# Kernel tuning notes

Hardware: AMD Instinct MI355X
Metric: run time of the kernel (lower is better)

The kernel has to match this reference:

```python
import jax, jax.numpy as jnp
import numpy as np

NUM_HEADS = 8
N_WIN = 8
TOPK = 4
DIM = 256


def setup_inputs() -> dict:
    key = jax.random.key(0)
    ks = jax.random.split(key, 5)
    B, T, H, W = 16, 16, 16, 16
    N = T * H * W
    x = jax.random.normal(ks[0], (B, N, DIM), dtype=jnp.float32)
    w_qkv = jax.random.normal(ks[1], (DIM, 3 * DIM), dtype=jnp.float32) * (DIM ** -0.5)
    b_qkv = jnp.zeros((3 * DIM,), dtype=jnp.float32)
    w_proj = jax.random.normal(ks[2], (DIM, DIM), dtype=jnp.float32) * (DIM ** -0.5)
    b_proj = jnp.zeros((DIM,), dtype=jnp.float32)
    return {"x": x, "w_qkv": w_qkv, "b_qkv": b_qkv, "w_proj": w_proj,
            "b_proj": b_proj, "T": T, "H": H, "W": W}


def reference(x, w_qkv, b_qkv, w_proj, b_proj, T, H, W):
    B, N, C = x.shape
    h = NUM_HEADS
    d = C // h
    scale = d ** -0.5
    S = H * W

    # qkv projection -> [3, B, T, h, S, d]
    qkv = (x.reshape(B, T, S, C) @ w_qkv + b_qkv).reshape(B, T, S, 3, h, d)
    qkv = jnp.transpose(qkv, (3, 0, 1, 4, 2, 5))
    q, k, v = qkv[0], qkv[1], qkv[2]

    n_win = N_WIN if S % N_WIN == 0 else S
    win = S // n_win
    qr = q.reshape(B, T, h, n_win, win, d)
    kr = k.reshape(B, T, h, n_win, win, d)
    vr = v.reshape(B, T, h, n_win, win, d)

    # spike-driven region features: sum over window tokens
    q_reg = qr.sum(axis=4)  # [B,T,h,n_win,d]
    k_reg = kr.sum(axis=4)
    sim = jnp.einsum('bthnd,bthmd->bthnm', q_reg, k_reg) * scale

    # mask out dead (non-firing) key regions
    activity = jnp.abs(kr).sum(axis=(4, 5))  # [B,T,h,n_win]
    act_mask = (activity > 1e-5).astype(sim.dtype)
    sim = sim + (1.0 - act_mask)[:, :, :, None, :] * -1e9

    tk = min(TOPK, n_win)
    _, idx = jax.lax.top_k(sim, tk)  # [B,T,h,n_win,tk]

    gidx = (idx[..., None] * win + jnp.arange(win)).reshape(B, T, h, n_win, tk * win)

    k_flat = kr.reshape(B, T, h, S, d)
    v_flat = vr.reshape(B, T, h, S, d)
    kg = jnp.take_along_axis(k_flat[:, :, :, None], gidx[..., None], axis=4)
    vg = jnp.take_along_axis(v_flat[:, :, :, None], gidx[..., None], axis=4)

    attn = jnp.einsum('bthnwd,bthngd->bthnwg', qr, kg) * scale
    attn = jax.nn.softmax(attn, axis=-1)
    out = jnp.einsum('bthnwg,bthngd->bthnwd', attn, vg)

    out = out.reshape(B, T, h, S, d).transpose(0, 1, 3, 2, 4).reshape(B, N, C)
    return out @ w_proj + b_proj
```

## Files before the change

### kernel.cpp

```cpp
#include <hip/hip_runtime.h>
#include <math.h>

constexpr int Bn   = 16;
constexpr int Tn   = 16;
constexpr int Sn   = 256;
constexpr int Cn   = 256;
constexpr int NH   = 8;
constexpr int HD   = 32;
constexpr int NW   = 8;
constexpr int WINW = 32;
constexpr float SCALE = 0.17677669529663687f;
constexpr float CEXP  = 0.2550756272475434f;

typedef __attribute__((ext_vector_type(8))) short bf16x8;
typedef __attribute__((ext_vector_type(4))) float f32x4;

__device__ inline float bf2f(unsigned short u) {
  return __uint_as_float(((unsigned int)u) << 16);
}
__device__ inline unsigned short f2bf(float f) {
  unsigned int u = __float_as_uint(f);
  u += 0x7FFFu + ((u >> 16) & 1u);
  return (unsigned short)(u >> 16);
}
__device__ inline unsigned int cvtpk_bf16(float lo, float hi) {
  unsigned int r;
  asm("v_cvt_pk_bf16_f32 %0, %1, %2" : "=v"(r) : "v"(lo), "v"(hi));
  return r;
}
__device__ inline float fast_exp2(float x) {
  float r;
  asm("v_exp_f32 %0, %1" : "=v"(r) : "v"(x));
  return r;
}
__device__ inline void gload16(const void* g, const void* l) {
  __builtin_amdgcn_global_load_lds(
      (const __attribute__((address_space(1))) void*)g,
      (__attribute__((address_space(3))) void*)l, 16, 0, 0);
}

__global__ __launch_bounds__(256) void k_prep(const float* __restrict__ x,
                                              const float* __restrict__ w_qkv,
                                              const float* __restrict__ w_proj,
                                              float* __restrict__ xs,
                                              unsigned short* __restrict__ xb,
                                              unsigned short* __restrict__ wtb,
                                              float* __restrict__ wtf,
                                              unsigned short* __restrict__ wpt) {
  const int blk = blockIdx.x;
  const int tid = threadIdx.x;
  if (blk < 2048) {
    const size_t row0 = (size_t)blk * 32;
    float acc = 0.f;
#pragma unroll
    for (int r = 0; r < 32; ++r) {
      const float val = x[(row0 + r) * Cn + tid];
      acc += val;
      xb[(row0 + r) * Cn + tid] = f2bf(val);
    }
    xs[(size_t)blk * Cn + tid] = acc;
  } else if (blk < 2816) {
    const int co = blk - 2048;
    const float val = w_qkv[(size_t)tid * 768 + co];
    wtf[(size_t)co * 256 + tid] = val;
    wtb[(size_t)co * 256 + tid] = f2bf(val);
  } else {
    const int co = blk - 2816;
    wpt[(size_t)co * 256 + tid] = f2bf(w_proj[(size_t)tid * 256 + co]);
  }
}

__global__ __launch_bounds__(256) void k_reg(const float* __restrict__ xs,
                                             const float* __restrict__ wtf,
                                             const float* __restrict__ bias,
                                             float* __restrict__ reg) {
  __shared__ __align__(16) float As[16][64];
  __shared__ __align__(16) float Bs[16][64];
  const int bx = blockIdx.x;
  const int by = blockIdx.y;
  const int tid = threadIdx.x;
  const int tx = tid & 15, ty = tid >> 4;
  const int row0 = by * 64, col0 = bx * 64;

  float acc[4][4] = {};

  for (int kk0 = 0; kk0 < 256; kk0 += 16) {
    const int m = tid >> 2, ks = (tid & 3) * 4;
    const float4 a4 = *reinterpret_cast<const float4*>(
        xs + (size_t)(row0 + m) * 256 + kk0 + ks);
    As[ks + 0][m] = a4.x; As[ks + 1][m] = a4.y;
    As[ks + 2][m] = a4.z; As[ks + 3][m] = a4.w;
    const float4 b4 = *reinterpret_cast<const float4*>(
        wtf + (size_t)(col0 + m) * 256 + kk0 + ks);
    Bs[ks + 0][m] = b4.x; Bs[ks + 1][m] = b4.y;
    Bs[ks + 2][m] = b4.z; Bs[ks + 3][m] = b4.w;
    __syncthreads();
#pragma unroll
    for (int kk = 0; kk < 16; ++kk) {
      const float4 a = *reinterpret_cast<const float4*>(&As[kk][ty * 4]);
      const float4 b = *reinterpret_cast<const float4*>(&Bs[kk][tx * 4]);
      const float av[4] = {a.x, a.y, a.z, a.w};
      const float bv[4] = {b.x, b.y, b.z, b.w};
#pragma unroll
      for (int i = 0; i < 4; ++i)
#pragma unroll
        for (int j = 0; j < 4; ++j) acc[i][j] = fmaf(av[i], bv[j], acc[i][j]);
    }
    __syncthreads();
  }

  const int colb = col0 + tx * 4;
  const float4 bia = *reinterpret_cast<const float4*>(bias + colb);
#pragma unroll
  for (int i = 0; i < 4; ++i) {
    const int row = row0 + ty * 4 + i;
    float4 o;
    o.x = acc[i][0] + 32.f * bia.x; o.y = acc[i][1] + 32.f * bia.y;
    o.z = acc[i][2] + 32.f * bia.z; o.w = acc[i][3] + 32.f * bia.w;
    *reinterpret_cast<float4*>(reg + (size_t)row * 512 + colb) = o;
  }
}

__global__ __launch_bounds__(64) void k_topk(const float* __restrict__ reg,
                                             int* __restrict__ idxout) {
  __shared__ float sq[8][32];
  __shared__ float sk[8][32];
  __shared__ float sim[8][8];
  const int bth = blockIdx.x;
  const int bt = bth >> 3, h = bth & 7;
  const int t = threadIdx.x;
#pragma unroll
  for (int n = 0; n < 8; ++n) {
    const size_t rb = (size_t)(bt * 8 + n) * 512 + h * 32;
    if (t < 32) sq[n][t] = reg[rb + t];
    else        sk[n][t - 32] = reg[rb + 256 + (t - 32)];
  }
  __syncthreads();
  {
    const int nn = t >> 3, m = t & 7;
    float s = 0.f;
#pragma unroll
    for (int i = 0; i < HD; ++i) s += sq[nn][i] * sk[m][i];
    sim[nn][m] = s;
  }
  __syncthreads();
  if (t < 8) {
    float vals[8];
#pragma unroll
    for (int m = 0; m < 8; ++m) vals[m] = sim[t][m];
#pragma unroll
    for (int j = 0; j < 4; ++j) {
      float best = -3.402823466e38f;
      int bi = 0;
#pragma unroll
      for (int m = 0; m < 8; ++m)
        if (vals[m] > best) { best = vals[m]; bi = m; }
      vals[bi] = -3.402823466e38f;
      idxout[((size_t)bth * 8 + t) * 4 + j] = bi;
    }
  }
}

__global__ __launch_bounds__(256) void k_qkv_mfma(
    const unsigned short* __restrict__ Xb,
    const unsigned short* __restrict__ Wt,
    const float* __restrict__ bias,
    unsigned short* __restrict__ q,
    unsigned short* __restrict__ k,
    unsigned short* __restrict__ v) {
  __shared__ short As[128 * 64];
  __shared__ short Bs[128 * 64];
  const int tid = threadIdx.x;
  const int wid = tid >> 6, lane = tid & 63;
  const int p = blockIdx.x;
  const int bidx = (p & 7) * 384 + (p >> 3);
  const int mt = bidx / 6, nt = bidx - mt * 6;
  const int row0 = mt * 128, col0 = nt * 128;
  const int wm = (wid >> 1) * 64, wn = (wid & 1) * 64;

  f32x4 acc[4][4] = {};

  const int lr = lane >> 3, lc = lane & 7;

  for (int kk0 = 0; kk0 < 256; kk0 += 64) {
#pragma unroll
    for (int j = 0; j < 4; ++j) {
      const int r = wid * 32 + j * 8 + lr;
      const int gsw = (lc ^ (r & 7)) * 8;
      gload16(Xb + (size_t)(row0 + r) * 256 + kk0 + gsw,
              (const char*)As + (wid * 32 + j * 8) * 128);
      gload16(Wt + (size_t)(col0 + r) * 256 + kk0 + gsw,
              (const char*)Bs + (wid * 32 + j * 8) * 128);
    }
    __syncthreads();

#pragma unroll
    for (int ks = 0; ks < 2; ++ks) {
      const int g = ks * 4 + (lane >> 4);
      bf16x8 af[4], bfr[4];
#pragma unroll
      for (int i = 0; i < 4; ++i) {
        const int rm = wm + i * 16 + (lane & 15);
        af[i] = *(const bf16x8*)((const char*)As + rm * 128 + 16 * (g ^ (rm & 7)));
        const int rn = wn + i * 16 + (lane & 15);
        bfr[i] = *(const bf16x8*)((const char*)Bs + rn * 128 + 16 * (g ^ (rn & 7)));
      }
#pragma unroll
      for (int i = 0; i < 4; ++i)
#pragma unroll
        for (int j = 0; j < 4; ++j)
          acc[i][j] = __builtin_amdgcn_mfma_f32_16x16x32_bf16(
              af[i], bfr[j], acc[i][j], 0, 0, 0);
    }
    __syncthreads();
  }

  const int cl = lane & 15, rg = lane >> 4;
#pragma unroll
  for (int j = 0; j < 4; ++j) {
    const int n = col0 + wn + j * 16 + cl;
    const float bia = bias[n];
    const int pp = n >> 8, hh = (n >> 5) & 7, dd = n & 31;
    unsigned short* dst = (pp == 0) ? q : (pp == 1) ? k : v;
#pragma unroll
    for (int i = 0; i < 4; ++i) {
      const int mbase = row0 + wm + i * 16 + rg * 4;
#pragma unroll
      for (int r = 0; r < 4; ++r) {
        const int m = mbase + r;
        const int bt = m >> 8, s = m & 255;
        dst[((size_t)(bt * NH + hh) * Sn + s) * HD + dd] = f2bf(acc[i][j][r] + bia);
      }
    }
  }
}

__global__ __launch_bounds__(256) void k_attn_mfma(
    const unsigned short* __restrict__ qb,
    const unsigned short* __restrict__ kb,
    const unsigned short* __restrict__ vb,
    const int* __restrict__ idx,
    unsigned short* __restrict__ ao) {
  __shared__ __align__(16) short kx[256 * 32];
  __shared__ __align__(16) short vt[32 * 264];
  __shared__ __align__(16) unsigned int pl[4][32 * 35];
  __shared__ float sbuf[4][32];
  const int bth = blockIdx.x;
  const int bt = bth >> 3, h = bth & 7;
  const int tid = threadIdx.x;
  const int wid = tid >> 6, l = tid & 63;
  const int g = l >> 4, q15 = l & 15;
  const unsigned short* kg = kb + (size_t)bth * 8192;
  const unsigned short* vg = vb + (size_t)bth * 8192;
  const unsigned short* qg = qb + (size_t)bth * 8192;

  {
    const int tloc = tid >> 2, cst = tid & 3;
#pragma unroll
    for (int it = 0; it < 4; ++it) {
      const int t = it * 64 + tloc;
      const int csrc = cst ^ ((t >> 1) & 3);
      gload16((const char*)kg + t * 64 + csrc * 16,
              (const char*)kx + it * 4096 + wid * 1024);
    }
  }
  {
    const int t = tid;
    unsigned short us[32];
#pragma unroll
    for (int i = 0; i < 4; ++i)
      *(int4*)(us + 8 * i) = ((const int4*)(vg + (size_t)t * 32))[i];
#pragma unroll
    for (int d = 0; d < 32; ++d) vt[d * 264 + t] = us[d];
  }
  __syncthreads();

#pragma unroll
  for (int ww = 0; ww < 2; ++ww) {
    const int wi = wid + ww * 4;
    const bf16x8 qf0 = *(const bf16x8*)(qg + (wi * 32 + q15) * 32 + g * 8);
    const bf16x8 qf1 = *(const bf16x8*)(qg + (wi * 32 + 16 + q15) * 32 + g * 8);
    const int4 s4 = *(const int4*)(idx + ((size_t)bth * 8 + wi) * 4);
    const int sel[4] = {s4.x, s4.y, s4.z, s4.w};

    f32x4 st[8][2] = {};
    __builtin_amdgcn_s_setprio(1);
#pragma unroll
    for (int mt = 0; mt < 8; ++mt) {
      const int t = sel[mt >> 1] * 32 + (mt & 1) * 16 + q15;
      const bf16x8 kf =
          *(const bf16x8*)((const char*)kx + t * 64 + (g ^ ((t >> 1) & 3)) * 16);
      st[mt][0] = __builtin_amdgcn_mfma_f32_16x16x32_bf16(kf, qf0, st[mt][0], 0, 0, 0);
      st[mt][1] = __builtin_amdgcn_mfma_f32_16x16x32_bf16(kf, qf1, st[mt][1], 0, 0, 0);
    }
    __builtin_amdgcn_s_setprio(0);

    float sm0 = 0.f, sm1 = 0.f;
#pragma unroll
    for (int mt = 0; mt < 8; ++mt)
#pragma unroll
      for (int r = 0; r < 4; ++r) {
        const float e0 = fast_exp2(st[mt][0][r] * CEXP);
        const float e1 = fast_exp2(st[mt][1][r] * CEXP);
        st[mt][0][r] = e0; sm0 += e0;
        st[mt][1][r] = e1; sm1 += e1;
      }
    sm0 += __shfl_xor(sm0, 16); sm0 += __shfl_xor(sm0, 32);
    sm1 += __shfl_xor(sm1, 16); sm1 += __shfl_xor(sm1, 32);
    sbuf[wid][q15] = sm0;
    sbuf[wid][16 + q15] = sm1;

    f32x4 oa[2][2] = {};
#pragma unroll
    for (int c = 0; c < 2; ++c) {
#pragma unroll
      for (int m3 = 0; m3 < 4; ++m3) {
        const int mt = c * 4 + m3;
        const int tl2 = m3 * 8 + 2 * g;
#pragma unroll
        for (int nt = 0; nt < 2; ++nt) {
          const int row = nt * 16 + q15;
          pl[wid][row * 35 + tl2]     = cvtpk_bf16(st[mt][nt][0], st[mt][nt][1]);
          pl[wid][row * 35 + tl2 + 1] = cvtpk_bf16(st[mt][nt][2], st[mt][nt][3]);
        }
      }
      __builtin_amdgcn_s_setprio(1);
#pragma unroll
      for (int a = 0; a < 2; ++a) {
        const bf16x8 pa0 = *(const bf16x8*)((const char*)&pl[wid][0] +
                                            q15 * 140 + (a * 32 + g * 8) * 2);
        const bf16x8 pa1 = *(const bf16x8*)((const char*)&pl[wid][0] +
                                            (16 + q15) * 140 + (a * 32 + g * 8) * 2);
        const int tv = sel[c * 2 + a] * 32 + g * 8;
#pragma unroll
        for (int nt = 0; nt < 2; ++nt) {
          const bf16x8 vf =
              *(const bf16x8*)((const char*)vt + (nt * 16 + q15) * 528 + tv * 2);
          oa[0][nt] = __builtin_amdgcn_mfma_f32_16x16x32_bf16(pa0, vf, oa[0][nt], 0, 0, 0);
          oa[1][nt] = __builtin_amdgcn_mfma_f32_16x16x32_bf16(pa1, vf, oa[1][nt], 0, 0, 0);
        }
      }
      __builtin_amdgcn_s_setprio(0);
    }

    const size_t rowbase = (size_t)bt * 256 + wi * 32;
#pragma unroll
    for (int mtO = 0; mtO < 2; ++mtO) {
      float inv[4];
#pragma unroll
      for (int r = 0; r < 4; ++r)
        inv[r] = __builtin_amdgcn_rcpf(sbuf[wid][mtO * 16 + g * 4 + r]);
#pragma unroll
      for (int nt = 0; nt < 2; ++nt)
#pragma unroll
        for (int r = 0; r < 4; ++r) {
          const size_t tok = rowbase + mtO * 16 + g * 4 + r;
          ao[tok * 256 + h * 32 + nt * 16 + q15] = f2bf(oa[mtO][nt][r] * inv[r]);
        }
    }
  }
}

__global__ __launch_bounds__(256) void k_proj_mfma(
    const unsigned short* __restrict__ AO,
    const unsigned short* __restrict__ Wp,
    const float* __restrict__ bias,
    float* __restrict__ out) {
  __shared__ short As[128 * 64];
  __shared__ short Bs[128 * 64];
  const int tid = threadIdx.x;
  const int wid = tid >> 6, lane = tid & 63;
  const int p = blockIdx.x;
  const int bidx = (p & 7) * 128 + (p >> 3);
  const int mt = bidx >> 1, nt = bidx & 1;
  const int row0 = mt * 128, col0 = nt * 128;
  const int wm = (wid >> 1) * 64, wn = (wid & 1) * 64;

  f32x4 acc[4][4] = {};
  const int lr = lane >> 3, lc = lane & 7;

  for (int kk0 = 0; kk0 < 256; kk0 += 64) {
#pragma unroll
    for (int j = 0; j < 4; ++j) {
      const int r = wid * 32 + j * 8 + lr;
      const int gsw = (lc ^ (r & 7)) * 8;
      gload16(AO + (size_t)(row0 + r) * 256 + kk0 + gsw,
              (const char*)As + (wid * 32 + j * 8) * 128);
      gload16(Wp + (size_t)(col0 + r) * 256 + kk0 + gsw,
              (const char*)Bs + (wid * 32 + j * 8) * 128);
    }
    __syncthreads();

#pragma unroll
    for (int ks = 0; ks < 2; ++ks) {
      const int g = ks * 4 + (lane >> 4);
      bf16x8 af[4], bfr[4];
#pragma unroll
      for (int i = 0; i < 4; ++i) {
        const int rm = wm + i * 16 + (lane & 15);
        af[i] = *(const bf16x8*)((const char*)As + rm * 128 + 16 * (g ^ (rm & 7)));
        const int rn = wn + i * 16 + (lane & 15);
        bfr[i] = *(const bf16x8*)((const char*)Bs + rn * 128 + 16 * (g ^ (rn & 7)));
      }
#pragma unroll
      for (int i = 0; i < 4; ++i)
#pragma unroll
        for (int j = 0; j < 4; ++j)
          acc[i][j] = __builtin_amdgcn_mfma_f32_16x16x32_bf16(
              af[i], bfr[j], acc[i][j], 0, 0, 0);
    }
    __syncthreads();
  }

  const int cl = lane & 15, rg = lane >> 4;
#pragma unroll
  for (int j = 0; j < 4; ++j) {
    const int n = col0 + wn + j * 16 + cl;
    const float bia = bias[n];
#pragma unroll
    for (int i = 0; i < 4; ++i) {
      const int mbase = row0 + wm + i * 16 + rg * 4;
#pragma unroll
      for (int r = 0; r < 4; ++r)
        out[(size_t)(mbase + r) * 256 + n] = acc[i][j][r] + bia;
    }
  }
}

extern "C" void kernel_launch(void* const* d_in, const int* in_sizes, int n_in,
                              void* d_out, int out_size, void* d_ws,
                              size_t ws_size, hipStream_t stream) {
  const float* x      = (const float*)d_in[0];
  const float* w_qkv  = (const float*)d_in[1];
  const float* b_qkv  = (const float*)d_in[2];
  const float* w_proj = (const float*)d_in[3];
  const float* b_proj = (const float*)d_in[4];
  float* out = (float*)d_out;

  char* ws = (char*)d_ws;
  unsigned short* xb  = (unsigned short*)(ws);
  unsigned short* ao  = (unsigned short*)(ws);
  unsigned short* q   = (unsigned short*)(ws + ((size_t)32 << 20));
  unsigned short* k   = (unsigned short*)(ws + ((size_t)64 << 20));
  unsigned short* v   = (unsigned short*)(ws + ((size_t)96 << 20));
  float*          xs  = (float*)(ws + ((size_t)128 << 20));
  unsigned short* wtb = (unsigned short*)(ws + ((size_t)131 << 20));
  unsigned short* wpt = (unsigned short*)(ws + ((size_t)131 << 20) + (512 << 10));
  float*          wtf = (float*)(ws + ((size_t)132 << 20));
  int*            idx = (int*)(ws + ((size_t)133 << 20));
  float*          regf= (float*)(ws + ((size_t)136 << 20));

  k_prep<<<3072, 256, 0, stream>>>(x, w_qkv, w_proj, xs, xb, wtb, wtf, wpt);
  k_reg<<<dim3(8, 32), 256, 0, stream>>>(xs, wtf, b_qkv, regf);
  k_topk<<<2048, 64, 0, stream>>>(regf, idx);
  k_qkv_mfma<<<3072, 256, 0, stream>>>(xb, wtb, b_qkv, q, k, v);
  k_attn_mfma<<<2048, 256, 0, stream>>>(q, k, v, idx, ao);
  k_proj_mfma<<<1024, 256, 0, stream>>>(ao, wpt, b_proj, out);
}
```

Measured before the change: 136.2 us.

## Fuse region GEMM with top-k, vectorize prep, double-buffer MFMA GEMM loads

Merges the region-feature GEMM and top-k selection into one kernel per (b,t) that keeps region q/k in shared memory. This removes one launch and the global round trip for the region features. The prep kernel now uses float4 loads and bf16x4 stores, combining partial row sums through shared memory. The QKV and projection MFMA GEMMs switch to double-buffered LDS so the next k-tile loads while the current one computes, at the cost of twice the LDS per block and possibly lower occupancy.

```diff
diff --git a/kernel.cpp b/kernel.cpp
--- a/kernel.cpp
+++ b/kernel.cpp
@@ -47,18 +47,27 @@
                                               unsigned short* __restrict__ wtb,
                                               float* __restrict__ wtf,
                                               unsigned short* __restrict__ wpt) {
+  __shared__ __align__(16) float psum[4][256];
   const int blk = blockIdx.x;
   const int tid = threadIdx.x;
   if (blk < 2048) {
     const size_t row0 = (size_t)blk * 32;
-    float acc = 0.f;
-#pragma unroll
-    for (int r = 0; r < 32; ++r) {
-      const float val = x[(row0 + r) * Cn + tid];
-      acc += val;
-      xb[(row0 + r) * Cn + tid] = f2bf(val);
-    }
-    xs[(size_t)blk * Cn + tid] = acc;
+    const int rg = tid >> 6, cg = tid & 63;
+    float4 s4 = {0.f, 0.f, 0.f, 0.f};
+#pragma unroll
+    for (int r = 0; r < 8; ++r) {
+      const size_t row = row0 + rg * 8 + r;
+      const float4 v = *(const float4*)(x + row * 256 + cg * 4);
+      s4.x += v.x; s4.y += v.y; s4.z += v.z; s4.w += v.w;
+      ushort4 u;
+      u.x = f2bf(v.x); u.y = f2bf(v.y); u.z = f2bf(v.z); u.w = f2bf(v.w);
+      *(ushort4*)(xb + row * 256 + cg * 4) = u;
+    }
+    *(float4*)&psum[rg][cg * 4] = s4;
+    __syncthreads();
+    const int c = tid;
+    xs[(size_t)blk * 256 + c] =
+        (psum[0][c] + psum[1][c]) + (psum[2][c] + psum[3][c]);
   } else if (blk < 2816) {
     const int co = blk - 2048;
     const float val = w_qkv[(size_t)tid * 768 + co];
@@ -70,84 +79,67 @@
   }
 }
 
-__global__ __launch_bounds__(256) void k_reg(const float* __restrict__ xs,
-                                             const float* __restrict__ wtf,
-                                             const float* __restrict__ bias,
-                                             float* __restrict__ reg) {
-  __shared__ __align__(16) float As[16][64];
-  __shared__ __align__(16) float Bs[16][64];
-  const int bx = blockIdx.x;
-  const int by = blockIdx.y;
+__global__ __launch_bounds__(256) void k_regtopk(const float* __restrict__ xs,
+                                                 const float* __restrict__ wtf,
+                                                 const float* __restrict__ bias,
+                                                 int* __restrict__ idxout) {
+  __shared__ __align__(16) float xl[8][256];
+  __shared__ __align__(16) float ql[8][256];
+  __shared__ __align__(16) float kl[8][256];
+  __shared__ float sim[8][8][8];
+  const int bt = blockIdx.x;
   const int tid = threadIdx.x;
-  const int tx = tid & 15, ty = tid >> 4;
-  const int row0 = by * 64, col0 = bx * 64;
-
-  float acc[4][4] = {};
-
-  for (int kk0 = 0; kk0 < 256; kk0 += 16) {
-    const int m = tid >> 2, ks = (tid & 3) * 4;
-    const float4 a4 = *reinterpret_cast<const float4*>(
-        xs + (size_t)(row0 + m) * 256 + kk0 + ks);
-    As[ks + 0][m] = a4.x; As[ks + 1][m] = a4.y;
-    As[ks + 2][m] = a4.z; As[ks + 3][m] = a4.w;
-    const float4 b4 = *reinterpret_cast<const float4*>(
-        wtf + (size_t)(col0 + m) * 256 + kk0 + ks);
-    Bs[ks + 0][m] = b4.x; Bs[ks + 1][m] = b4.y;
-    Bs[ks + 2][m] = b4.z; Bs[ks + 3][m] = b4.w;
-    __syncthreads();
-#pragma unroll
-    for (int kk = 0; kk < 16; ++kk) {
-      const float4 a = *reinterpret_cast<const float4*>(&As[kk][ty * 4]);
-      const float4 b = *reinterpret_cast<const float4*>(&Bs[kk][tx * 4]);
-      const float av[4] = {a.x, a.y, a.z, a.w};
-      const float bv[4] = {b.x, b.y, b.z, b.w};
-#pragma unroll
-      for (int i = 0; i < 4; ++i)
-#pragma unroll
-        for (int j = 0; j < 4; ++j) acc[i][j] = fmaf(av[i], bv[j], acc[i][j]);
-    }
-    __syncthreads();
-  }
-
-  const int colb = col0 + tx * 4;
-  const float4 bia = *reinterpret_cast<const float4*>(bias + colb);
-#pragma unroll
-  for (int i = 0; i < 4; ++i) {
-    const int row = row0 + ty * 4 + i;
-    float4 o;
-    o.x = acc[i][0] + 32.f * bia.x; o.y = acc[i][1] + 32.f * bia.y;
-    o.z = acc[i][2] + 32.f * bia.z; o.w = acc[i][3] + 32.f * bia.w;
-    *reinterpret_cast<float4*>(reg + (size_t)row * 512 + colb) = o;
-  }
-}
-
-__global__ __launch_bounds__(64) void k_topk(const float* __restrict__ reg,
-                                             int* __restrict__ idxout) {
-  __shared__ float sq[8][32];
-  __shared__ float sk[8][32];
-  __shared__ float sim[8][8];
-  const int bth = blockIdx.x;
-  const int bt = bth >> 3, h = bth & 7;
-  const int t = threadIdx.x;
-#pragma unroll
-  for (int n = 0; n < 8; ++n) {
-    const size_t rb = (size_t)(bt * 8 + n) * 512 + h * 32;
-    if (t < 32) sq[n][t] = reg[rb + t];
-    else        sk[n][t - 32] = reg[rb + 256 + (t - 32)];
+  {
+    const float4* src = (const float4*)(xs + (size_t)bt * 2048);
+    float4* dst = (float4*)&xl[0][0];
+    dst[tid] = src[tid];
+    dst[tid + 256] = src[tid + 256];
   }
   __syncthreads();
   {
-    const int nn = t >> 3, m = t & 7;
-    float s = 0.f;
-#pragma unroll
-    for (int i = 0; i < HD; ++i) s += sq[nn][i] * sk[m][i];
-    sim[nn][m] = s;
+    float accq[8] = {}, acck[8] = {};
+    const float4* wq = (const float4*)(wtf + (size_t)tid * 256);
+    const float4* wk = (const float4*)(wtf + (size_t)(256 + tid) * 256);
+#pragma unroll 4
+    for (int i = 0; i < 64; ++i) {
+      const float4 a = wq[i];
+      const float4 b = wk[i];
+#pragma unroll
+      for (int n = 0; n < 8; ++n) {
+        const float4 xv = *(const float4*)&xl[n][i * 4];
+        accq[n] = fmaf(xv.x, a.x,
+                  fmaf(xv.y, a.y, fmaf(xv.z, a.z, fmaf(xv.w, a.w, accq[n]))));
+        acck[n] = fmaf(xv.x, b.x,
+                  fmaf(xv.y, b.y, fmaf(xv.z, b.z, fmaf(xv.w, b.w, acck[n]))));
+      }
+    }
+    const float bq = 32.f * bias[tid];
+    const float bk = 32.f * bias[256 + tid];
+#pragma unroll
+    for (int n = 0; n < 8; ++n) {
+      ql[n][tid] = accq[n] + bq;
+      kl[n][tid] = acck[n] + bk;
+    }
   }
   __syncthreads();
-  if (t < 8) {
+  {
+    const int h = tid >> 5, n = (tid >> 2) & 7, m0 = (tid & 3) * 2;
+#pragma unroll
+    for (int mm = 0; mm < 2; ++mm) {
+      const int m = m0 + mm;
+      float s = 0.f;
+#pragma unroll
+      for (int d = 0; d < 32; ++d)
+        s = fmaf(ql[n][h * 32 + d], kl[m][h * 32 + d], s);
+      sim[h][n][m] = s;
+    }
+  }
+  __syncthreads();
+  if (tid < 64) {
+    const int h = tid >> 3, n = tid & 7;
     float vals[8];
 #pragma unroll
-    for (int m = 0; m < 8; ++m) vals[m] = sim[t][m];
+    for (int m = 0; m < 8; ++m) vals[m] = sim[h][n][m];
 #pragma unroll
     for (int j = 0; j < 4; ++j) {
       float best = -3.402823466e38f;
@@ -156,7 +148,7 @@
       for (int m = 0; m < 8; ++m)
         if (vals[m] > best) { best = vals[m]; bi = m; }
       vals[bi] = -3.402823466e38f;
-      idxout[((size_t)bth * 8 + t) * 4 + j] = bi;
+      idxout[(((size_t)bt * 8 + h) * 8 + n) * 4 + j] = bi;
     }
   }
 }
@@ -168,8 +160,8 @@
     unsigned short* __restrict__ q,
     unsigned short* __restrict__ k,
     unsigned short* __restrict__ v) {
-  __shared__ short As[128 * 64];
-  __shared__ short Bs[128 * 64];
+  __shared__ short As[2][128 * 64];
+  __shared__ short Bs[2][128 * 64];
   const int tid = threadIdx.x;
   const int wid = tid >> 6, lane = tid & 63;
   const int p = blockIdx.x;
@@ -179,21 +171,28 @@
   const int wm = (wid >> 1) * 64, wn = (wid & 1) * 64;
 
   f32x4 acc[4][4] = {};
-
   const int lr = lane >> 3, lc = lane & 7;
 
-  for (int kk0 = 0; kk0 < 256; kk0 += 64) {
-#pragma unroll
-    for (int j = 0; j < 4; ++j) {
-      const int r = wid * 32 + j * 8 + lr;
-      const int gsw = (lc ^ (r & 7)) * 8;
-      gload16(Xb + (size_t)(row0 + r) * 256 + kk0 + gsw,
-              (const char*)As + (wid * 32 + j * 8) * 128);
-      gload16(Wt + (size_t)(col0 + r) * 256 + kk0 + gsw,
-              (const char*)Bs + (wid * 32 + j * 8) * 128);
-    }
-    __syncthreads();
-
+#define QSTAGE(kk0, b)                                                     \
+  {                                                                        \
+    _Pragma("unroll") for (int j = 0; j < 4; ++j) {                        \
+      const int r = wid * 32 + j * 8 + lr;                                 \
+      const int gsw = (lc ^ (r & 7)) * 8;                                  \
+      gload16(Xb + (size_t)(row0 + r) * 256 + (kk0) + gsw,                 \
+              (const char*)&As[b][0] + (wid * 32 + j * 8) * 128);          \
+      gload16(Wt + (size_t)(col0 + r) * 256 + (kk0) + gsw,                 \
+              (const char*)&Bs[b][0] + (wid * 32 + j * 8) * 128);          \
+    }                                                                      \
+  }
+
+  QSTAGE(0, 0)
+  asm volatile("s_waitcnt vmcnt(0)" ::: "memory");
+  __builtin_amdgcn_s_barrier();
+
+#pragma unroll
+  for (int t = 0; t < 4; ++t) {
+    const int cur = t & 1;
+    if (t < 3) QSTAGE((t + 1) * 64, cur ^ 1)
 #pragma unroll
     for (int ks = 0; ks < 2; ++ks) {
       const int g = ks * 4 + (lane >> 4);
@@ -201,9 +200,11 @@
 #pragma unroll
       for (int i = 0; i < 4; ++i) {
         const int rm = wm + i * 16 + (lane & 15);
-        af[i] = *(const bf16x8*)((const char*)As + rm * 128 + 16 * (g ^ (rm & 7)));
+        af[i] = *(const bf16x8*)((const char*)&As[cur][0] + rm * 128 +
+                                 16 * (g ^ (rm & 7)));
         const int rn = wn + i * 16 + (lane & 15);
-        bfr[i] = *(const bf16x8*)((const char*)Bs + rn * 128 + 16 * (g ^ (rn & 7)));
+        bfr[i] = *(const bf16x8*)((const char*)&Bs[cur][0] + rn * 128 +
+                                  16 * (g ^ (rn & 7)));
       }
 #pragma unroll
       for (int i = 0; i < 4; ++i)
@@ -212,7 +213,8 @@
           acc[i][j] = __builtin_amdgcn_mfma_f32_16x16x32_bf16(
               af[i], bfr[j], acc[i][j], 0, 0, 0);
     }
-    __syncthreads();
+    asm volatile("s_waitcnt vmcnt(0)" ::: "memory");
+    __builtin_amdgcn_s_barrier();
   }
 
   const int cl = lane & 15, rg = lane >> 4;
@@ -366,8 +368,8 @@
     const unsigned short* __restrict__ Wp,
     const float* __restrict__ bias,
     float* __restrict__ out) {
-  __shared__ short As[128 * 64];
-  __shared__ short Bs[128 * 64];
+  __shared__ short As[2][128 * 64];
+  __shared__ short Bs[2][128 * 64];
   const int tid = threadIdx.x;
   const int wid = tid >> 6, lane = tid & 63;
   const int p = blockIdx.x;
@@ -379,18 +381,26 @@
   f32x4 acc[4][4] = {};
   const int lr = lane >> 3, lc = lane & 7;
 
-  for (int kk0 = 0; kk0 < 256; kk0 += 64) {
-#pragma unroll
-    for (int j = 0; j < 4; ++j) {
-      const int r = wid * 32 + j * 8 + lr;
-      const int gsw = (lc ^ (r & 7)) * 8;
-      gload16(AO + (size_t)(row0 + r) * 256 + kk0 + gsw,
-              (const char*)As + (wid * 32 + j * 8) * 128);
-      gload16(Wp + (size_t)(col0 + r) * 256 + kk0 + gsw,
-              (const char*)Bs + (wid * 32 + j * 8) * 128);
-    }
-    __syncthreads();
-
+#define PSTAGE(kk0, b)                                                     \
+  {                                                                        \
+    _Pragma("unroll") for (int j = 0; j < 4; ++j) {                        \
+      const int r = wid * 32 + j * 8 + lr;                                 \
+      const int gsw = (lc ^ (r & 7)) * 8;                                  \
+      gload16(AO + (size_t)(row0 + r) * 256 + (kk0) + gsw,                 \
+              (const char*)&As[b][0] + (wid * 32 + j * 8) * 128);          \
+      gload16(Wp + (size_t)(col0 + r) * 256 + (kk0) + gsw,                 \
+              (const char*)&Bs[b][0] + (wid * 32 + j * 8) * 128);          \
+    }                                                                      \
+  }
+
+  PSTAGE(0, 0)
+  asm volatile("s_waitcnt vmcnt(0)" ::: "memory");
+  __builtin_amdgcn_s_barrier();
+
+#pragma unroll
+  for (int t = 0; t < 4; ++t) {
+    const int cur = t & 1;
+    if (t < 3) PSTAGE((t + 1) * 64, cur ^ 1)
 #pragma unroll
     for (int ks = 0; ks < 2; ++ks) {
       const int g = ks * 4 + (lane >> 4);
@@ -398,9 +408,11 @@
 #pragma unroll
       for (int i = 0; i < 4; ++i) {
         const int rm = wm + i * 16 + (lane & 15);
-        af[i] = *(const bf16x8*)((const char*)As + rm * 128 + 16 * (g ^ (rm & 7)));
+        af[i] = *(const bf16x8*)((const char*)&As[cur][0] + rm * 128 +
+                                 16 * (g ^ (rm & 7)));
         const int rn = wn + i * 16 + (lane & 15);
-        bfr[i] = *(const bf16x8*)((const char*)Bs + rn * 128 + 16 * (g ^ (rn & 7)));
+        bfr[i] = *(const bf16x8*)((const char*)&Bs[cur][0] + rn * 128 +
+                                  16 * (g ^ (rn & 7)));
       }
 #pragma unroll
       for (int i = 0; i < 4; ++i)
@@ -409,7 +421,8 @@
           acc[i][j] = __builtin_amdgcn_mfma_f32_16x16x32_bf16(
               af[i], bfr[j], acc[i][j], 0, 0, 0);
     }
-    __syncthreads();
+    asm volatile("s_waitcnt vmcnt(0)" ::: "memory");
+    __builtin_amdgcn_s_barrier();
   }
 
   const int cl = lane & 15, rg = lane >> 4;
@@ -448,11 +461,9 @@
   unsigned short* wpt = (unsigned short*)(ws + ((size_t)131 << 20) + (512 << 10));
   float*          wtf = (float*)(ws + ((size_t)132 << 20));
   int*            idx = (int*)(ws + ((size_t)133 << 20));
-  float*          regf= (float*)(ws + ((size_t)136 << 20));
 
   k_prep<<<3072, 256, 0, stream>>>(x, w_qkv, w_proj, xs, xb, wtb, wtf, wpt);
-  k_reg<<<dim3(8, 32), 256, 0, stream>>>(xs, wtf, b_qkv, regf);
-  k_topk<<<2048, 64, 0, stream>>>(regf, idx);
+  k_regtopk<<<256, 256, 0, stream>>>(xs, wtf, b_qkv, idx);
   k_qkv_mfma<<<3072, 256, 0, stream>>>(xb, wtb, b_qkv, q, k, v);
   k_attn_mfma<<<2048, 256, 0, stream>>>(q, k, v, idx, ao);
   k_proj_mfma<<<1024, 256, 0, stream>>>(ao, wpt, b_proj, out);
```

Measured after the change: 139.1 us. 2.1% more time.
